# Optimization experiments

Measured on AMD Instinct MI355X. Metric: run time of the kernel, lower is better.

The kernel has to match this reference:

```python
import jax, jax.numpy as jnp
import numpy as np

N_TOK = 4096   # total packed tokens
HID   = 2048   # n_hidden
NH    = 16     # n_head
HD    = HID // NH  # head_dim = 128
SEQ   = 1024   # per-sequence length (equal-length packing)
NSEQ  = N_TOK // SEQ
EPS   = 1e-6


def setup_inputs() -> dict:
    key = jax.random.key(0)
    ks = jax.random.split(key, 5)
    x = jax.random.normal(ks[0], (N_TOK, HID), jnp.float32)
    Wqkv = jax.random.normal(ks[1], (3 * HID, HID), jnp.float32) * (HID ** -0.5)
    Wo = jax.random.normal(ks[2], (HID, HID), jnp.float32) * (HID ** -0.5)
    gate_w = jax.random.normal(ks[3], (NH, HID), jnp.float32) * 0.02
    gate_b = jnp.zeros((NH,), jnp.float32)
    norm_w = jnp.ones((HD,), jnp.float32)  # RMSNorm weight over head_dim
    # rotary caches: [rope_cache_len, head_dim//2]
    pos = jnp.arange(SEQ, dtype=jnp.float32)
    inv_freq = 1.0 / (10000.0 ** (jnp.arange(0, HD, 2, dtype=jnp.float32) / HD))
    ang = pos[:, None] * inv_freq[None, :]
    cos_cache = jnp.cos(ang)
    sin_cache = jnp.sin(ang)
    cu_seqlens = (jnp.arange(NSEQ + 1, dtype=jnp.int32) * SEQ)
    position_ids = jnp.tile(jnp.arange(SEQ, dtype=jnp.int64), NSEQ)
    return {
        "x": x, "Wqkv": Wqkv, "Wo": Wo, "gate_w": gate_w, "gate_b": gate_b,
        "norm_w": norm_w, "cos_cache": cos_cache, "sin_cache": sin_cache,
        "cu_seqlens": cu_seqlens, "max_seqlen": SEQ, "position_ids": position_ids,
    }


def reference(x, Wqkv, Wo, gate_w, gate_b, norm_w, cos_cache, sin_cache,
              cu_seqlens, max_seqlen, position_ids):
    # fused QKV projection -> [N, 3, H, D]
    qkv = (x @ Wqkv.T).reshape(N_TOK, 3, NH, HD)
    cos = cos_cache[position_ids][:, None, :]  # [N, 1, D//2]
    sin = sin_cache[position_ids][:, None, :]

    def rope(t):  # t: [N, H, D]
        d = HD // 2
        x1, x2 = t[..., :d], t[..., d:]
        return jnp.concatenate([x1 * cos + x2 * sin, -x1 * sin + x2 * cos], axis=-1)

    def rmsnorm(t):  # per-head RMSNorm over D
        return t * jax.lax.rsqrt(jnp.mean(t * t, axis=-1, keepdims=True) + EPS) * norm_w

    q = rmsnorm(rope(qkv[:, 0]))
    k = rmsnorm(rope(qkv[:, 1]))
    v = qkv[:, 2]

    # equal-length packed sequences -> reshape to [B, S, H, D]
    B, S = NSEQ, max_seqlen
    q = q.reshape(B, S, NH, HD)
    k = k.reshape(B, S, NH, HD)
    v = v.reshape(B, S, NH, HD)

    scores = jnp.einsum("bqhd,bkhd->bhqk", q, k) * (HD ** -0.5)
    causal = jnp.tril(jnp.ones((S, S), bool))
    scores = jnp.where(causal, scores, jnp.float32(-1e30))
    probs = jax.nn.softmax(scores, axis=-1)
    attn_out = jnp.einsum("bhqk,bkhd->bqhd", probs, v).reshape(N_TOK, NH, HD)

    gate = jax.nn.sigmoid(x @ gate_w.T + gate_b)[:, :, None]  # [N, H, 1]
    out = (attn_out * gate).reshape(N_TOK, HID)
    return out @ Wo.T
```

## Files before the change

### kernel.cpp

```cpp
#include <hip/hip_runtime.h>
#include <hip/hip_bf16.h>
#include <math.h>

#define N_TOK 4096
#define HID   2048
#define NH    16
#define HD    128
#define SEQ   1024
#define NSEQ  4
#define QKVN  (3*HID)
#define KSPLIT (3*HID)

typedef __bf16 bf16x8 __attribute__((ext_vector_type(8)));
typedef float  f32x4  __attribute__((ext_vector_type(4)));
typedef unsigned short ushort8v __attribute__((ext_vector_type(8)));

#define MFMA16(a,b,c) __builtin_amdgcn_mfma_f32_16x16x32_bf16(a,b,c,0,0,0)

__device__ __forceinline__ ushort bf16_rn(float f) {
  unsigned u = __float_as_uint(f);
  return (ushort)((u + 0x7FFFu + ((u >> 16) & 1u)) >> 16);
}
__device__ __forceinline__ float bf16_tof(ushort h) {
  return __uint_as_float(((unsigned)h) << 16);
}
__device__ __forceinline__ void gload16(const void* g, void* l) {
  __builtin_amdgcn_global_load_lds(
      (const __attribute__((address_space(1))) void*)g,
      (__attribute__((address_space(3))) void*)l, 16, 0, 0);
}

#define CFENCE asm volatile("" ::: "memory")
#define BARR do { __builtin_amdgcn_sched_barrier(0); CFENCE; \
                  __builtin_amdgcn_s_barrier(); CFENCE; \
                  __builtin_amdgcn_sched_barrier(0); } while (0)
#define VMCNT4 do { __builtin_amdgcn_sched_barrier(0); \
                    asm volatile("s_waitcnt vmcnt(4)" ::: "memory"); } while (0)

__global__ __launch_bounds__(256)
void split_bf16(const float* __restrict__ src, ushort* __restrict__ dst,
                int total4, int amode) {
  for (int idx = blockIdx.x * 256 + threadIdx.x; idx < total4;
       idx += gridDim.x * 256) {
    const int r = idx >> 9, kq = idx & 511;
    float4 v = ((const float4*)src)[idx];
    float f[4] = {v.x, v.y, v.z, v.w};
    ushort h[4], lo[4];
    #pragma unroll
    for (int j = 0; j < 4; ++j) {
      h[j]  = bf16_rn(f[j]);
      lo[j] = bf16_rn(f[j] - bf16_tof(h[j]));
    }
    ushort4 hv = make_ushort4(h[0], h[1], h[2], h[3]);
    ushort4 lv = make_ushort4(lo[0], lo[1], lo[2], lo[3]);
    ushort* row = dst + (size_t)r * KSPLIT + kq * 4;
    *(ushort4*)(row)        = hv;
    *(ushort4*)(row + 2048) = amode ? hv : lv;
    *(ushort4*)(row + 4096) = amode ? lv : hv;
  }
}

__global__ __launch_bounds__(512, 2)
void gemm256(const ushort* __restrict__ A, const ushort* __restrict__ B,
             float* __restrict__ C, int M, int N, int K) {
  extern __shared__ ushort lds[];
  const int nx = gridDim.x;
  const int nwg = nx * gridDim.y;
  const int bid = blockIdx.y * nx + blockIdx.x;
  const int cpx = nwg >> 3;
  const int swz = (bid & 7) * cpx + (bid >> 3);
  const int bx = swz % nx, by = swz / nx;
  const int m0 = by * 256, n0 = bx * 256;
  const int tid = threadIdx.x;
  const int w = tid >> 6, l = tid & 63;
  const int wm = w >> 2, wn = w & 3;
  const int fr = l & 15, kc = l >> 4;
  const int cx = (kc ^ ((fr >> 1) & 3)) * 8;
  const int aoff = (wm * 128 + fr) * 32 + cx;
  const int boff = 16384 + (wn * 64 + fr) * 32 + cx;
  const int tr0 = tid >> 2;
  const int q0c = tid & 3;
  const int wub = (tid & 448) * 8;
  const int NTILE = K >> 6;

  auto stage = [&](int bufus, int kt, int s) {
    const int koe = kt * 64 + s * 32;
    #pragma unroll
    for (int i = 0; i < 2; ++i) {
      const int tr = i * 128 + tr0;
      const int gq = (q0c ^ ((tr >> 1) & 3)) * 8;
      gload16(A + (size_t)(m0 + tr) * K + koe + gq,
              &lds[bufus + s * 8192 + i * 8192 / 2 * 0 + (i * 512) * 8 + wub]);
    }
    #pragma unroll
    for (int i = 0; i < 2; ++i) {
      const int tr = i * 128 + tr0;
      const int gq = (q0c ^ ((tr >> 1) & 3)) * 8;
      gload16(B + (size_t)(n0 + tr) * K + koe + gq,
              &lds[bufus + 16384 + s * 8192 + (i * 512) * 8 + wub]);
    }
  };
  auto lda4 = [&](bf16x8* dst, int cb, int s, int mbase) {
    #pragma unroll
    for (int m = 0; m < 4; ++m)
      dst[m] = *(const bf16x8*)&lds[cb + s * 8192 + aoff + (mbase + m) * 512];
  };
  auto ldb4 = [&](bf16x8* dst, int cb, int s) {
    #pragma unroll
    for (int n = 0; n < 4; ++n)
      dst[n] = *(const bf16x8*)&lds[cb + s * 8192 + boff + n * 512];
  };

  f32x4 acc[8][4];
  #pragma unroll
  for (int m = 0; m < 8; ++m)
    #pragma unroll
    for (int n = 0; n < 4; ++n)
      acc[m][n] = (f32x4){0.f, 0.f, 0.f, 0.f};

  auto mm = [&](bf16x8* av_, bf16x8* bv_, int mbase) {
    __builtin_amdgcn_s_setprio(1);
    #pragma unroll
    for (int m = 0; m < 4; ++m)
      #pragma unroll
      for (int n = 0; n < 4; ++n)
        acc[mbase + m][n] = MFMA16(av_[m], bv_[n], acc[mbase + m][n]);
    __builtin_amdgcn_s_setprio(0);
  };

  stage(0, 0, 0);
  stage(0, 0, 1);
  VMCNT4;
  BARR;

  for (int T = 0; T < NTILE; ++T) {
    const int cb = (T & 1) << 15;
    const int nb = 32768 - cb;
    const bool st = (T + 1) < NTILE;
    bf16x8 a0[4], b0[4], a1[4];
    lda4(a0, cb, 0, 0);
    ldb4(b0, cb, 0);
    if (st) stage(nb, T + 1, 0);
    BARR;
    mm(a0, b0, 0);
    BARR;
    lda4(a1, cb, 0, 4);
    VMCNT4;
    BARR;
    mm(a1, b0, 4);
    BARR;
    lda4(a0, cb, 1, 0);
    ldb4(b0, cb, 1);
    if (st) stage(nb, T + 1, 1);
    BARR;
    mm(a0, b0, 0);
    BARR;
    lda4(a1, cb, 1, 4);
    VMCNT4;
    BARR;
    mm(a1, b0, 4);
    BARR;
  }

  const int crow = (l >> 4) * 4, ccol = l & 15;
  #pragma unroll
  for (int m = 0; m < 8; ++m)
    #pragma unroll
    for (int n = 0; n < 4; ++n) {
      #pragma unroll
      for (int j = 0; j < 4; ++j)
        C[(size_t)(m0 + wm * 128 + m * 16 + crow + j) * N +
          (n0 + wn * 64 + n * 16 + ccol)] = acc[m][n][j];
    }
}

__global__ __launch_bounds__(256)
void gemm_bf16_nt(const ushort* __restrict__ A, const ushort* __restrict__ B,
                  float* __restrict__ C, int M, int N, int K) {
  __shared__ ushort As[128 * 32];
  __shared__ ushort Bs[128 * 32];
  const int nx = gridDim.x;
  const int nwg = nx * gridDim.y;
  const int bid = blockIdx.y * nx + blockIdx.x;
  const int cpx = nwg >> 3;
  const int swz = (bid & 7) * cpx + (bid >> 3);
  const int bx = swz % nx, by = swz / nx;
  const int tid = threadIdx.x;
  const int w = tid >> 6, l = tid & 63;
  const int wm = w >> 1, wn = w & 1;
  const int m0 = by * 128, n0 = bx * 128;
  const int lr = l & 15;
  const int ko = (l >> 4) * 8;
  const int srow = l >> 2;
  const int scol = (l & 3) * 8;

  f32x4 acc[4][4];
  #pragma unroll
  for (int m = 0; m < 4; ++m)
    #pragma unroll
    for (int n = 0; n < 4; ++n)
      acc[m][n] = (f32x4){0.f, 0.f, 0.f, 0.f};

  for (int k0 = 0; k0 < K; k0 += 32) {
    #pragma unroll
    for (int i = 0; i < 2; ++i) {
      const int rbase = w * 32 + i * 16;
      const ushort* ga = A + (size_t)(m0 + rbase + srow) * K + k0 + scol;
      const ushort* gb = B + (size_t)(n0 + rbase + srow) * K + k0 + scol;
      gload16(ga, &As[rbase * 32]);
      gload16(gb, &Bs[rbase * 32]);
    }
    __syncthreads();
    bf16x8 av[4], bv[4];
    #pragma unroll
    for (int m = 0; m < 4; ++m)
      av[m] = *(const bf16x8*)&As[(wm * 64 + m * 16 + lr) * 32 + ko];
    #pragma unroll
    for (int n = 0; n < 4; ++n)
      bv[n] = *(const bf16x8*)&Bs[(wn * 64 + n * 16 + lr) * 32 + ko];
    #pragma unroll
    for (int m = 0; m < 4; ++m)
      #pragma unroll
      for (int n = 0; n < 4; ++n)
        acc[m][n] = MFMA16(av[m], bv[n], acc[m][n]);
    __syncthreads();
  }
  const int crow = (l >> 4) * 4, ccol = l & 15;
  #pragma unroll
  for (int m = 0; m < 4; ++m)
    #pragma unroll
    for (int n = 0; n < 4; ++n) {
      #pragma unroll
      for (int j = 0; j < 4; ++j)
        C[(size_t)(m0 + wm * 64 + m * 16 + crow + j) * N +
          (n0 + wn * 64 + n * 16 + ccol)] = acc[m][n][j];
    }
}

__global__ __launch_bounds__(256)
void rope_split(const float* __restrict__ qkv, const float* __restrict__ norm_w,
                const float* __restrict__ cosc, const float* __restrict__ sinc,
                const int* __restrict__ cu,
                ushort* __restrict__ Qsp, ushort* __restrict__ Ksp) {
  const int wid  = blockIdx.x * 4 + (threadIdx.x >> 6);
  const int lane = threadIdx.x & 63;
  const int t   = wid >> 5;
  const int rem = wid & 31;
  const int s   = rem >> 4;
  const int h   = rem & 15;
  const int pos = t - cu[t >> 10];
  const float* p = qkv + (size_t)t * QKVN + s * HID + h * HD;
  float x1 = p[lane], x2 = p[lane + 64];
  float c  = cosc[pos * 64 + lane];
  float sn = sinc[pos * 64 + lane];
  float y1 = x1 * c + x2 * sn;
  float y2 = x2 * c - x1 * sn;
  float ss = y1 * y1 + y2 * y2;
  #pragma unroll
  for (int o = 32; o > 0; o >>= 1) ss += __shfl_xor(ss, o, 64);
  float r = rsqrtf(ss * (1.0f / 128.0f) + 1e-6f);
  const float sc = s ? 1.0f : 0.08838834764831845f;
  float o1 = y1 * r * norm_w[lane] * sc;
  float o2 = y2 * r * norm_w[lane + 64] * sc;
  ushort h1 = bf16_rn(o1), l1 = bf16_rn(o1 - bf16_tof(h1));
  ushort h2 = bf16_rn(o2), l2 = bf16_rn(o2 - bf16_tof(h2));
  char* db = (char*)((s ? Ksp : Qsp) + ((size_t)t * NH + h) * 256);
  const int b0 = (lane * 2) ^ ((t & 7) << 4);
  *(ushort*)(db + b0)       = h1;
  *(ushort*)(db + 128 + b0) = h2;
  *(ushort*)(db + 256 + b0) = l1;
  *(ushort*)(db + 384 + b0) = l2;
}

__global__ __launch_bounds__(256)
void v_split_t(const float* __restrict__ qkv, ushort* __restrict__ Vt) {
  __shared__ float Vb[64][133];
  const int kt = blockIdx.x, bh = blockIdx.y;
  const int b = bh >> 4, h = bh & 15;
  const int tid = threadIdx.x;
  {
    const int k = tid >> 5, dm = (tid & 31) * 4;
    const float* src = qkv + (size_t)(b * SEQ + kt * 64) * QKVN + 2 * HID + h * HD;
    #pragma unroll
    for (int i = 0; i < 8; ++i) {
      float4 v = *(const float4*)(src + (size_t)(i * 8 + k) * QKVN + dm);
      Vb[i * 8 + k][dm]     = v.x;
      Vb[i * 8 + k][dm + 1] = v.y;
      Vb[i * 8 + k][dm + 2] = v.z;
      Vb[i * 8 + k][dm + 3] = v.w;
    }
  }
  __syncthreads();
  const int c  = tid & 7;
  const int d0 = tid >> 3;
  char* base = (char*)Vt + (size_t)bh * 256 * 2048;
  #pragma unroll
  for (int it = 0; it < 4; ++it) {
    const int d = d0 + it * 32;
    ushort8v vh, vl;
    #pragma unroll
    for (int j = 0; j < 8; ++j) {
      float f = Vb[c * 8 + j][d];
      ushort hh = bf16_rn(f);
      vh[j] = hh;
      vl[j] = bf16_rn(f - bf16_tof(hh));
    }
    const int cc = (c ^ (d & 7)) * 16;
    *(ushort8v*)(base + (size_t)d * 2048 + kt * 128 + cc)        = vh;
    *(ushort8v*)(base + (size_t)(128 + d) * 2048 + kt * 128 + cc) = vl;
  }
}

__global__ __launch_bounds__(256)
void gate_kernel(const float* __restrict__ x, const float* __restrict__ gw,
                 const float* __restrict__ gb, float* __restrict__ gate) {
  __shared__ float xs[HID];
  const int t = blockIdx.x, tid = threadIdx.x;
  *(float4*)&xs[tid * 8]     = *(const float4*)&x[(size_t)t * HID + tid * 8];
  *(float4*)&xs[tid * 8 + 4] = *(const float4*)&x[(size_t)t * HID + tid * 8 + 4];
  __syncthreads();
  const int h = tid >> 4, i = tid & 15;
  const float* w  = gw + (size_t)h * HID + i * 128;
  const float* xx = xs + i * 128;
  float sum = 0.f;
  #pragma unroll
  for (int j = 0; j < 128; j += 4) {
    float4 wv = *(const float4*)(w + j);
    float4 xv = *(const float4*)(xx + j);
    sum += wv.x * xv.x + wv.y * xv.y + wv.z * xv.z + wv.w * xv.w;
  }
  sum += __shfl_xor(sum, 8, 64);
  sum += __shfl_xor(sum, 4, 64);
  sum += __shfl_xor(sum, 2, 64);
  sum += __shfl_xor(sum, 1, 64);
  if (i == 0) gate[t * NH + h] = 1.f / (1.f + __expf(-(sum + gb[h])));
}

__global__ __launch_bounds__(256, 1)
void attn_mfma(const ushort* __restrict__ Qsp, const ushort* __restrict__ Ksp,
               const ushort* __restrict__ Vtg, const float* __restrict__ gate,
               float* __restrict__ og) {
  __shared__ ushort Qs[64 * 256];
  __shared__ ushort Ks[64 * 256];
  __shared__ ushort Vs[256 * 64];
  __shared__ float  SP[64 * 66];
  __shared__ float  cf[64];
  const int bh = blockIdx.x, b = bh >> 4, h = bh & 15;
  const int qt = (int)gridDim.y - 1 - (int)blockIdx.y;
  const int tid = threadIdx.x;
  const int w = tid >> 6, l = tid & 63;
  const int wm = w >> 1, wn = w & 1;
  const int fr = l & 15;
  const int fk = (l >> 4) * 16;
  const int swr = (fr & 7) << 4;
  const int crow = (l >> 4) * 4, ccol = l & 15;
  const int sr = tid >> 2, so = tid & 3;

  {
    const char* qg = (const char*)Qsp + ((size_t)(b * SEQ + qt * 64) * 16 + h) * 512
                     + (size_t)w * 131072 + (size_t)(l >> 5) * 8192 + (l & 31) * 16;
    char* qd = (char*)Qs + w * 8192;
    #pragma unroll
    for (int i = 0; i < 8; ++i) gload16(qg + i * 16384, qd + i * 1024);
  }
  const char* kg = (const char*)Ksp + ((size_t)(b * SEQ) * 16 + h) * 512
                   + (size_t)w * 131072 + (size_t)(l >> 5) * 8192 + (l & 31) * 16;
  const char* vg = (const char*)Vtg + ((size_t)bh * 256 + w * 64 + (l >> 3)) * 2048
                   + (l & 7) * 16;
  char* kd = (char*)Ks + w * 8192;
  char* vd = (char*)Vs + w * 8192;

  f32x4 acc_o[2][4];
  #pragma unroll
  for (int mi = 0; mi < 2; ++mi)
    #pragma unroll
    for (int ni = 0; ni < 4; ++ni)
      acc_o[mi][ni] = (f32x4){0.f, 0.f, 0.f, 0.f};
  float m_run = -INFINITY, l_run = 0.f;

  for (int kt = 0; kt <= qt; ++kt) {
    #pragma unroll
    for (int i = 0; i < 8; ++i) gload16(kg + i * 16384, kd + i * 1024);
    #pragma unroll
    for (int i = 0; i < 8; ++i) gload16(vg + i * 16384, vd + i * 1024);
    kg += 524288;
    vg += 128;
    __syncthreads();

    f32x4 acc_s[2][2];
    #pragma unroll
    for (int mi = 0; mi < 2; ++mi)
      #pragma unroll
      for (int ni = 0; ni < 2; ++ni)
        acc_s[mi][ni] = (f32x4){0.f, 0.f, 0.f, 0.f};
    #pragma unroll
    for (int term = 0; term < 3; ++term) {
      const int qo = (term == 2) ? 256 : 0;
      const int ko2 = (term == 1) ? 256 : 0;
      #pragma unroll
      for (int ks = 0; ks < 4; ++ks) {
        const int ia = (qo + ks * 64 + fk) ^ swr;
        const int ib = (ko2 + ks * 64 + fk) ^ swr;
        bf16x8 a0 = *(const bf16x8*)((const char*)Qs + (wm * 32 + fr) * 512 + ia);
        bf16x8 a1 = *(const bf16x8*)((const char*)Qs + (wm * 32 + 16 + fr) * 512 + ia);
        bf16x8 b0 = *(const bf16x8*)((const char*)Ks + (wn * 32 + fr) * 512 + ib);
        bf16x8 b1 = *(const bf16x8*)((const char*)Ks + (wn * 32 + 16 + fr) * 512 + ib);
        acc_s[0][0] = MFMA16(a0, b0, acc_s[0][0]);
        acc_s[0][1] = MFMA16(a0, b1, acc_s[0][1]);
        acc_s[1][0] = MFMA16(a1, b0, acc_s[1][0]);
        acc_s[1][1] = MFMA16(a1, b1, acc_s[1][1]);
      }
    }
    #pragma unroll
    for (int mi = 0; mi < 2; ++mi)
      #pragma unroll
      for (int ni = 0; ni < 2; ++ni)
        #pragma unroll
        for (int j = 0; j < 4; ++j)
          SP[(wm * 32 + mi * 16 + crow + j) * 66 + wn * 32 + ni * 16 + ccol] =
              acc_s[mi][ni][j];
    __syncthreads();

    float s[16];
    #pragma unroll
    for (int j = 0; j < 16; ++j) s[j] = SP[sr * 66 + so * 16 + j];
    __syncthreads();

    {
      if (kt == qt) {
        #pragma unroll
        for (int j = 0; j < 16; ++j)
          if (so * 16 + j > sr) s[j] = -INFINITY;
      }
      float mx = -INFINITY;
      #pragma unroll
      for (int j = 0; j < 16; ++j) mx = fmaxf(mx, s[j]);
      mx = fmaxf(mx, __shfl_xor(mx, 1, 64));
      mx = fmaxf(mx, __shfl_xor(mx, 2, 64));
      float mnew = fmaxf(m_run, mx);
      float corr = __expf(m_run - mnew);
      float p[16];
      float ls = 0.f;
      #pragma unroll
      for (int j = 0; j < 16; ++j) { p[j] = __expf(s[j] - mnew); ls += p[j]; }
      ls += __shfl_xor(ls, 1, 64);
      ls += __shfl_xor(ls, 2, 64);
      l_run = l_run * corr + ls;
      m_run = mnew;
      char* prow = (char*)SP + sr * 256;
      const int swp = (sr & 7) << 4;
      #pragma unroll
      for (int half = 0; half < 2; ++half) {
        ushort8v vh, vl;
        #pragma unroll
        for (int j = 0; j < 8; ++j) {
          float pv = p[half * 8 + j];
          ushort hh = bf16_rn(pv);
          vh[j] = hh;
          vl[j] = bf16_rn(pv - bf16_tof(hh));
        }
        const int cb = (so * 32 + half * 16) ^ swp;
        *(ushort8v*)(prow + cb)       = vh;
        *(ushort8v*)(prow + 128 + cb) = vl;
      }
      if (so == 0) cf[sr] = corr;
    }
    __syncthreads();

    {
      float cl[8];
      #pragma unroll
      for (int mi = 0; mi < 2; ++mi)
        #pragma unroll
        for (int j = 0; j < 4; ++j)
          cl[mi * 4 + j] = cf[wm * 32 + mi * 16 + crow + j];
      #pragma unroll
      for (int mi = 0; mi < 2; ++mi)
        #pragma unroll
        for (int ni = 0; ni < 4; ++ni)
          #pragma unroll
          for (int j = 0; j < 4; ++j)
            acc_o[mi][ni][j] *= cl[mi * 4 + j];
      #pragma unroll
      for (int term = 0; term < 3; ++term) {
        const int po = (term == 2) ? 128 : 0;
        const int vo = (term == 1) ? 128 : 0;
        #pragma unroll
        for (int ks = 0; ks < 2; ++ks) {
          const int ip = (ks * 64 + fk) ^ swr;
          bf16x8 pa0 = *(const bf16x8*)((const char*)SP + (wm * 32 + fr) * 256 + po + ip);
          bf16x8 pa1 = *(const bf16x8*)((const char*)SP + (wm * 32 + 16 + fr) * 256 + po + ip);
          #pragma unroll
          for (int ni = 0; ni < 4; ++ni) {
            const int dr = vo + wn * 64 + ni * 16 + fr;
            bf16x8 vv = *(const bf16x8*)((const char*)Vs + dr * 128 + ((ks * 64 + fk) ^ swr));
            acc_o[0][ni] = MFMA16(pa0, vv, acc_o[0][ni]);
            acc_o[1][ni] = MFMA16(pa1, vv, acc_o[1][ni]);
          }
        }
      }
    }
    __syncthreads();
  }

  if (so == 0) {
    const int t = b * SEQ + qt * 64 + sr;
    cf[sr] = gate[t * NH + h] / l_run;
  }
  __syncthreads();
  {
    float rf[8];
    #pragma unroll
    for (int mi = 0; mi < 2; ++mi)
      #pragma unroll
      for (int j = 0; j < 4; ++j)
        rf[mi * 4 + j] = cf[wm * 32 + mi * 16 + crow + j];
    #pragma unroll
    for (int mi = 0; mi < 2; ++mi)
      #pragma unroll
      for (int ni = 0; ni < 4; ++ni)
        #pragma unroll
        for (int j = 0; j < 4; ++j)
          og[(size_t)(b * SEQ + qt * 64 + wm * 32 + mi * 16 + crow + j) * HID
             + h * HD + wn * 64 + ni * 16 + ccol] = acc_o[mi][ni][j] * rf[mi * 4 + j];
  }
}

extern "C" void kernel_launch(void* const* d_in, const int* in_sizes, int n_in,
                              void* d_out, int out_size, void* d_ws, size_t ws_size,
                              hipStream_t stream) {
  const float* x    = (const float*)d_in[0];
  const float* Wqkv = (const float*)d_in[1];
  const float* Wo   = (const float*)d_in[2];
  const float* gw   = (const float*)d_in[3];
  const float* gb   = (const float*)d_in[4];
  const float* nw   = (const float*)d_in[5];
  const float* cosc = (const float*)d_in[6];
  const float* sinc = (const float*)d_in[7];
  const int*   cu   = (const int*)d_in[8];
  float* out = (float*)d_out;

  float*  qkv  = (float*)d_ws;
  float*  attn = qkv + (size_t)N_TOK * QKVN;
  float*  gate = attn + (size_t)N_TOK * HID;
  ushort* Abuf = (ushort*)(gate + (size_t)N_TOK * NH);
  ushort* Bbuf = Abuf + (size_t)N_TOK * KSPLIT;
  ushort* Qsp = Abuf;
  ushort* Ksp = Bbuf;
  ushort* Vt  = Bbuf + (size_t)N_TOK * NH * 256;

  (void)hipFuncSetAttribute((const void*)gemm256,
                            hipFuncAttributeMaxDynamicSharedMemorySize, 131072);

  split_bf16<<<2048, 256, 0, stream>>>(x,    Abuf, N_TOK * HID / 4, 1);
  split_bf16<<<2048, 256, 0, stream>>>(Wqkv, Bbuf, QKVN * HID / 4, 0);
  gemm256<<<dim3(QKVN / 256, N_TOK / 256), 512, 131072, stream>>>(
      Abuf, Bbuf, qkv, N_TOK, QKVN, KSPLIT);

  rope_split<<<dim3(N_TOK * 2 * NH / 4), 256, 0, stream>>>(qkv, nw, cosc, sinc,
                                                           cu, Qsp, Ksp);
  v_split_t<<<dim3(16, 64), 256, 0, stream>>>(qkv, Vt);
  gate_kernel<<<dim3(N_TOK), 256, 0, stream>>>(x, gw, gb, gate);

  attn_mfma<<<dim3(NSEQ * NH, SEQ / 64), 256, 0, stream>>>(Qsp, Ksp, Vt, gate, attn);

  split_bf16<<<2048, 256, 0, stream>>>(attn, Abuf, N_TOK * HID / 4, 1);
  split_bf16<<<2048, 256, 0, stream>>>(Wo,   Bbuf, HID * HID / 4, 0);
  gemm_bf16_nt<<<dim3(HID / 128, N_TOK / 128), 256, 0, stream>>>(
      Abuf, Bbuf, out, N_TOK, HID, KSPLIT);
}
```

Baseline: 875.7 us.

## Fuse bf16 hi/lo split into attention epilogue and pipeline output GEMM

The attention kernel now writes its gated output directly as the split bf16 hi/hi/lo row layout the output projection consumes, so the fp32 attention buffer and its separate split pass go away. The output projection switches from a simple single-buffered 128x128 GEMM to a 256x128-tile, double-buffered, swizzled-LDS kernel with async global-to-LDS loads and priority hints. Buffer layout moves Q out of Abuf to avoid aliasing. This risks scattered 2-byte stores in the attention epilogue and higher register/LDS pressure in the new GEMM.

```diff
diff --git a/kernel.cpp b/kernel.cpp
--- a/kernel.cpp
+++ b/kernel.cpp
@@ -36,6 +36,8 @@
                   __builtin_amdgcn_sched_barrier(0); } while (0)
 #define VMCNT4 do { __builtin_amdgcn_sched_barrier(0); \
                     asm volatile("s_waitcnt vmcnt(4)" ::: "memory"); } while (0)
+#define VMCNT3 do { __builtin_amdgcn_sched_barrier(0); \
+                    asm volatile("s_waitcnt vmcnt(3)" ::: "memory"); } while (0)
 
 __global__ __launch_bounds__(256)
 void split_bf16(const float* __restrict__ src, ushort* __restrict__ dst,
@@ -90,14 +92,14 @@
       const int tr = i * 128 + tr0;
       const int gq = (q0c ^ ((tr >> 1) & 3)) * 8;
       gload16(A + (size_t)(m0 + tr) * K + koe + gq,
-              &lds[bufus + s * 8192 + i * 8192 / 2 * 0 + (i * 512) * 8 + wub]);
+              &lds[bufus + s * 8192 + i * 4096 + wub]);
     }
     #pragma unroll
     for (int i = 0; i < 2; ++i) {
       const int tr = i * 128 + tr0;
       const int gq = (q0c ^ ((tr >> 1) & 3)) * 8;
       gload16(B + (size_t)(n0 + tr) * K + koe + gq,
-              &lds[bufus + 16384 + s * 8192 + (i * 512) * 8 + wub]);
+              &lds[bufus + 16384 + s * 8192 + i * 4096 + wub]);
     }
   };
   auto lda4 = [&](bf16x8* dst, int cb, int s, int mbase) {
@@ -174,25 +176,55 @@
     }
 }
 
-__global__ __launch_bounds__(256)
-void gemm_bf16_nt(const ushort* __restrict__ A, const ushort* __restrict__ B,
-                  float* __restrict__ C, int M, int N, int K) {
-  __shared__ ushort As[128 * 32];
-  __shared__ ushort Bs[128 * 32];
+__global__ __launch_bounds__(512, 2)
+void gemm256_bn128(const ushort* __restrict__ A, const ushort* __restrict__ B,
+                   float* __restrict__ C, int M, int N, int K) {
+  extern __shared__ ushort lds[];
   const int nx = gridDim.x;
   const int nwg = nx * gridDim.y;
   const int bid = blockIdx.y * nx + blockIdx.x;
   const int cpx = nwg >> 3;
   const int swz = (bid & 7) * cpx + (bid >> 3);
   const int bx = swz % nx, by = swz / nx;
+  const int m0 = by * 256, n0 = bx * 128;
   const int tid = threadIdx.x;
   const int w = tid >> 6, l = tid & 63;
   const int wm = w >> 1, wn = w & 1;
-  const int m0 = by * 128, n0 = bx * 128;
-  const int lr = l & 15;
-  const int ko = (l >> 4) * 8;
-  const int srow = l >> 2;
-  const int scol = (l & 3) * 8;
+  const int fr = l & 15, kc = l >> 4;
+  const int cx = (kc ^ ((fr >> 1) & 3)) * 8;
+  const int aoff = (wm * 64 + fr) * 32 + cx;
+  const int tr0 = tid >> 2;
+  const int q0c = tid & 3;
+  const int wub = (tid & 448) * 8;
+  const int NTILE = K >> 6;
+
+  auto stage = [&](int bufus, int kt, int s) {
+    const int koe = kt * 64 + s * 32;
+    #pragma unroll
+    for (int i = 0; i < 2; ++i) {
+      const int tr = i * 128 + tr0;
+      const int gq = (q0c ^ ((tr >> 1) & 3)) * 8;
+      gload16(A + (size_t)(m0 + tr) * K + koe + gq,
+              &lds[bufus + s * 8192 + i * 4096 + wub]);
+    }
+    {
+      const int tr = tr0;
+      const int gq = (q0c ^ ((tr >> 1) & 3)) * 8;
+      gload16(B + (size_t)(n0 + tr) * K + koe + gq,
+              &lds[bufus + 16384 + s * 4096 + wub]);
+    }
+  };
+  auto lda2 = [&](bf16x8* dst, int cb, int s, int mbase) {
+    #pragma unroll
+    for (int m = 0; m < 2; ++m)
+      dst[m] = *(const bf16x8*)&lds[cb + s * 8192 + aoff + (mbase + m) * 512];
+  };
+  auto ldb4 = [&](bf16x8* dst, int cb, int s) {
+    #pragma unroll
+    for (int n = 0; n < 4; ++n)
+      dst[n] = *(const bf16x8*)&lds[cb + 16384 + s * 4096 +
+                                    (wn * 64 + n * 16 + fr) * 32 + cx];
+  };
 
   f32x4 acc[4][4];
   #pragma unroll
@@ -201,30 +233,50 @@
     for (int n = 0; n < 4; ++n)
       acc[m][n] = (f32x4){0.f, 0.f, 0.f, 0.f};
 
-  for (int k0 = 0; k0 < K; k0 += 32) {
-    #pragma unroll
-    for (int i = 0; i < 2; ++i) {
-      const int rbase = w * 32 + i * 16;
-      const ushort* ga = A + (size_t)(m0 + rbase + srow) * K + k0 + scol;
-      const ushort* gb = B + (size_t)(n0 + rbase + srow) * K + k0 + scol;
-      gload16(ga, &As[rbase * 32]);
-      gload16(gb, &Bs[rbase * 32]);
-    }
-    __syncthreads();
-    bf16x8 av[4], bv[4];
-    #pragma unroll
-    for (int m = 0; m < 4; ++m)
-      av[m] = *(const bf16x8*)&As[(wm * 64 + m * 16 + lr) * 32 + ko];
-    #pragma unroll
-    for (int n = 0; n < 4; ++n)
-      bv[n] = *(const bf16x8*)&Bs[(wn * 64 + n * 16 + lr) * 32 + ko];
-    #pragma unroll
-    for (int m = 0; m < 4; ++m)
+  auto mm = [&](bf16x8* av_, bf16x8* bv_, int mbase) {
+    __builtin_amdgcn_s_setprio(1);
+    #pragma unroll
+    for (int m = 0; m < 2; ++m)
       #pragma unroll
       for (int n = 0; n < 4; ++n)
-        acc[m][n] = MFMA16(av[m], bv[n], acc[m][n]);
-    __syncthreads();
-  }
+        acc[mbase + m][n] = MFMA16(av_[m], bv_[n], acc[mbase + m][n]);
+    __builtin_amdgcn_s_setprio(0);
+  };
+
+  stage(0, 0, 0);
+  stage(0, 0, 1);
+  VMCNT3;
+  BARR;
+
+  for (int T = 0; T < NTILE; ++T) {
+    const int cb = (T & 1) ? 24576 : 0;
+    const int nb = 24576 - cb;
+    const bool st = (T + 1) < NTILE;
+    bf16x8 a0[2], b0[4], a1[2];
+    lda2(a0, cb, 0, 0);
+    ldb4(b0, cb, 0);
+    if (st) stage(nb, T + 1, 0);
+    BARR;
+    mm(a0, b0, 0);
+    BARR;
+    lda2(a1, cb, 0, 2);
+    VMCNT3;
+    BARR;
+    mm(a1, b0, 2);
+    BARR;
+    lda2(a0, cb, 1, 0);
+    ldb4(b0, cb, 1);
+    if (st) stage(nb, T + 1, 1);
+    BARR;
+    mm(a0, b0, 0);
+    BARR;
+    lda2(a1, cb, 1, 2);
+    VMCNT3;
+    BARR;
+    mm(a1, b0, 2);
+    BARR;
+  }
+
   const int crow = (l >> 4) * 4, ccol = l & 15;
   #pragma unroll
   for (int m = 0; m < 4; ++m)
@@ -339,7 +391,7 @@
 __global__ __launch_bounds__(256, 1)
 void attn_mfma(const ushort* __restrict__ Qsp, const ushort* __restrict__ Ksp,
                const ushort* __restrict__ Vtg, const float* __restrict__ gate,
-               float* __restrict__ og) {
+               ushort* __restrict__ Aout) {
   __shared__ ushort Qs[64 * 256];
   __shared__ ushort Ks[64 * 256];
   __shared__ ushort Vs[256 * 64];
@@ -518,11 +570,21 @@
     #pragma unroll
     for (int mi = 0; mi < 2; ++mi)
       #pragma unroll
-      for (int ni = 0; ni < 4; ++ni)
+      for (int j = 0; j < 4; ++j) {
+        const int trow = b * SEQ + qt * 64 + wm * 32 + mi * 16 + crow + j;
+        ushort* rp = Aout + (size_t)trow * KSPLIT;
+        const float rfv = rf[mi * 4 + j];
         #pragma unroll
-        for (int j = 0; j < 4; ++j)
-          og[(size_t)(b * SEQ + qt * 64 + wm * 32 + mi * 16 + crow + j) * HID
-             + h * HD + wn * 64 + ni * 16 + ccol] = acc_o[mi][ni][j] * rf[mi * 4 + j];
+        for (int ni = 0; ni < 4; ++ni) {
+          const float v = acc_o[mi][ni][j] * rfv;
+          const ushort hh = bf16_rn(v);
+          const ushort ll = bf16_rn(v - bf16_tof(hh));
+          const int col = h * HD + wn * 64 + ni * 16 + ccol;
+          rp[col]        = hh;
+          rp[col + 2048] = hh;
+          rp[col + 4096] = ll;
+        }
+      }
   }
 }
 
@@ -541,16 +603,17 @@
   float* out = (float*)d_out;
 
   float*  qkv  = (float*)d_ws;
-  float*  attn = qkv + (size_t)N_TOK * QKVN;
-  float*  gate = attn + (size_t)N_TOK * HID;
+  ushort* Qsp  = (ushort*)(qkv + (size_t)N_TOK * QKVN);
+  float*  gate = (float*)(Qsp + (size_t)N_TOK * NH * 256);
   ushort* Abuf = (ushort*)(gate + (size_t)N_TOK * NH);
   ushort* Bbuf = Abuf + (size_t)N_TOK * KSPLIT;
-  ushort* Qsp = Abuf;
-  ushort* Ksp = Bbuf;
-  ushort* Vt  = Bbuf + (size_t)N_TOK * NH * 256;
+  ushort* Ksp  = Bbuf;
+  ushort* Vt   = Bbuf + (size_t)N_TOK * NH * 256;
 
   (void)hipFuncSetAttribute((const void*)gemm256,
                             hipFuncAttributeMaxDynamicSharedMemorySize, 131072);
+  (void)hipFuncSetAttribute((const void*)gemm256_bn128,
+                            hipFuncAttributeMaxDynamicSharedMemorySize, 98304);
 
   split_bf16<<<2048, 256, 0, stream>>>(x,    Abuf, N_TOK * HID / 4, 1);
   split_bf16<<<2048, 256, 0, stream>>>(Wqkv, Bbuf, QKVN * HID / 4, 0);
@@ -562,10 +625,9 @@
   v_split_t<<<dim3(16, 64), 256, 0, stream>>>(qkv, Vt);
   gate_kernel<<<dim3(N_TOK), 256, 0, stream>>>(x, gw, gb, gate);
 
-  attn_mfma<<<dim3(NSEQ * NH, SEQ / 64), 256, 0, stream>>>(Qsp, Ksp, Vt, gate, attn);
-
-  split_bf16<<<2048, 256, 0, stream>>>(attn, Abuf, N_TOK * HID / 4, 1);
-  split_bf16<<<2048, 256, 0, stream>>>(Wo,   Bbuf, HID * HID / 4, 0);
-  gemm_bf16_nt<<<dim3(HID / 128, N_TOK / 128), 256, 0, stream>>>(
+  attn_mfma<<<dim3(NSEQ * NH, SEQ / 64), 256, 0, stream>>>(Qsp, Ksp, Vt, gate, Abuf);
+
+  split_bf16<<<2048, 256, 0, stream>>>(Wo, Bbuf, HID * HID / 4, 0);
+  gemm256_bn128<<<dim3(HID / 128, N_TOK / 256), 512, 98304, stream>>>(
       Abuf, Bbuf, out, N_TOK, HID, KSPLIT);
 }
```

Result: faster. 846.7 us (-3.3%).
